# Kernel tuning notes

Measured on AMD Instinct MI355X. Metric: run time of the kernel, lower is better.

The kernel has to match this reference:

```python
import jax, jax.numpy as jnp
import numpy as np

N = 100_000   # num nodes
E = 1_600_000 # num edges
C = 128       # in_channels == hidden_channels
L = 3         # n_layers
EPS = 1e-5    # BatchNorm eps (torch default)


def bn(h, g, b, m, v):
    # BatchNorm1d in eval mode: running stats
    return (h - m) * jax.lax.rsqrt(v + EPS) * g + b


def sage_layer(h, src, dst, Wl_i, bl_i, Wr_i):
    # mean aggregation of incoming neighbor messages (PyG SAGEConv default)
    msg = h[src]                                                   # [E, C] gather
    agg = jax.ops.segment_sum(msg, dst, num_segments=N)            # [N, C]
    cnt = jax.ops.segment_sum(jnp.ones((src.shape[0],), h.dtype), dst, num_segments=N)
    agg = agg / jnp.maximum(cnt, 1.0)[:, None]
    return agg @ Wl_i + bl_i + h @ Wr_i                            # lin_l(agg) + lin_r(x)


def setup_inputs() -> dict:
    key = jax.random.key(0)
    ks = jax.random.split(key, 32)
    s = 0.05
    d = {}
    d["x"] = jax.random.normal(ks[0], (N, C), jnp.float32)
    d["edge_index"] = jax.random.randint(ks[1], (2, E), 0, N, dtype=jnp.int32)
    d["batch_size"] = 50_000
    d["Wl"] = jax.random.normal(ks[2], (L, C, C), jnp.float32) * s
    d["bl"] = jax.random.normal(ks[3], (L, C), jnp.float32) * s
    d["Wr"] = jax.random.normal(ks[4], (L, C, C), jnp.float32) * s
    d["bn_g"] = jax.random.uniform(ks[5], (L, C), jnp.float32, 0.5, 1.5)
    d["bn_b"] = jax.random.normal(ks[6], (L, C), jnp.float32) * s
    d["bn_m"] = jax.random.normal(ks[7], (L, C), jnp.float32) * s
    d["bn_v"] = jax.random.uniform(ks[8], (L, C), jnp.float32, 0.5, 1.5)
    d["cW1"] = jax.random.normal(ks[9], (C, C), jnp.float32) * s
    d["cb1"] = jax.random.normal(ks[10], (C,), jnp.float32) * s
    d["cg1"] = jax.random.uniform(ks[11], (C,), jnp.float32, 0.5, 1.5)
    d["cbe1"] = jax.random.normal(ks[12], (C,), jnp.float32) * s
    d["cm1"] = jax.random.normal(ks[13], (C,), jnp.float32) * s
    d["cv1"] = jax.random.uniform(ks[14], (C,), jnp.float32, 0.5, 1.5)
    d["cW2"] = jax.random.normal(ks[15], (C, C // 2), jnp.float32) * s
    d["cb2"] = jax.random.normal(ks[16], (C // 2,), jnp.float32) * s
    d["cg2"] = jax.random.uniform(ks[17], (C // 2,), jnp.float32, 0.5, 1.5)
    d["cbe2"] = jax.random.normal(ks[18], (C // 2,), jnp.float32) * s
    d["cm2"] = jax.random.normal(ks[19], (C // 2,), jnp.float32) * s
    d["cv2"] = jax.random.uniform(ks[20], (C // 2,), jnp.float32, 0.5, 1.5)
    d["cW3"] = jax.random.normal(ks[21], (C // 2, 1), jnp.float32) * s
    d["cb3"] = jax.random.normal(ks[22], (1,), jnp.float32) * s
    return d


def reference(x, edge_index, batch_size, Wl, bl, Wr, bn_g, bn_b, bn_m, bn_v,
              cW1, cb1, cg1, cbe1, cm1, cv1,
              cW2, cb2, cg2, cbe2, cm2, cv2, cW3, cb3):
    src, dst = edge_index[0], edge_index[1]
    h = x
    for l in range(L):  # small fixed layer count
        h = bn(jax.nn.relu(sage_layer(h, src, dst, Wl[l], bl[l], Wr[l])),
               bn_g[l], bn_b[l], bn_m[l], bn_v[l])
        # dropout is identity in eval mode
    h = h[:batch_size]                                             # [B, C] seed nodes
    h = jax.nn.relu(bn(h @ cW1 + cb1, cg1, cbe1, cm1, cv1))
    h = jax.nn.relu(bn(h @ cW2 + cb2, cg2, cbe2, cm2, cv2))
    return (h @ cW3 + cb3)[:, 0]                                   # [B]
```

## Files before the change

### kernel.cpp

```cpp
#include <hip/hip_runtime.h>

#define N_NODES 100000
#define N_EDGES 1600000
#define CDIM    128
#define BATCH   50000
#define NLAYERS 3
#define EPS_BN  1e-5f
#define LPAD    136

#define NBUCK   512
#define BW      196
#define EPB     4096
#define NEB     ((N_EDGES + EPB - 1) / EPB)
#define EBCAP   3584

#define ECAP    704

#define BBLK3   ((BATCH + 31) / 32)

typedef __attribute__((ext_vector_type(8))) short short8;
typedef __attribute__((ext_vector_type(4))) float floatx4;
typedef __attribute__((ext_vector_type(2))) float floatx2;

__device__ __forceinline__ unsigned short f2bf(float f) {
    unsigned int u = __float_as_uint(f);
    u = u + 0x7FFFu + ((u >> 16) & 1u);
    return (unsigned short)(u >> 16);
}
__device__ __forceinline__ unsigned int pk2(float lo, float hi) {
    return (unsigned int)f2bf(lo) | ((unsigned int)f2bf(hi) << 16);
}

__device__ __forceinline__ floatx2 fp8x2_lo(unsigned int u) {
    return __builtin_amdgcn_cvt_pk_f32_fp8((int)u, false);
}
__device__ __forceinline__ floatx2 fp8x2_hi(unsigned int u) {
    return __builtin_amdgcn_cvt_pk_f32_fp8((int)u, true);
}
__device__ __forceinline__ unsigned int f32x4_to_fp8(float f0, float f1, float f2, float f3) {
    int w = __builtin_amdgcn_cvt_pk_fp8_f32(f0, f1, 0, false);
    w = __builtin_amdgcn_cvt_pk_fp8_f32(f2, f3, w, true);
    return (unsigned int)w;
}

__device__ __forceinline__ void acc8(uint2 u, floatx2& a01, floatx2& a23,
                                     floatx2& a45, floatx2& a67) {
    a01 = a01 + fp8x2_lo(u.x);
    a23 = a23 + fp8x2_hi(u.x);
    a45 = a45 + fp8x2_lo(u.y);
    a67 = a67 + fp8x2_hi(u.y);
}
__device__ __forceinline__ void acc8w(uint2 u, float w, floatx2& a01, floatx2& a23,
                                      floatx2& a45, floatx2& a67) {
    floatx2 wv; wv.x = w; wv.y = w;
    a01 = fp8x2_lo(u.x) * wv + a01;
    a23 = fp8x2_hi(u.x) * wv + a23;
    a45 = fp8x2_lo(u.y) * wv + a45;
    a67 = fp8x2_hi(u.y) * wv + a67;
}

#define OFF_HB0   6400000
#define OFF_HB1   12800000
#define OFF_SC    19200000
#define OFF_RP    19201152
#define OFF_BCNT  19301184
#define OFF_ELIST 19302752
#define OFF_EBUF  20902752
#define OFF_WCAT  22737760
#define OFF_WH1   22786912
#define OFF_WH2   22795104
#define OFF_XQ    22800000
#define OFF_HQ0   26000000
#define OFF_HQ1   29200000

#define XBLK 12500
#define WBLK 384
#define HBLK 96
#define SETUP_BLKS (XBLK + WBLK + HBLK + 1)
__global__ __launch_bounds__(256) void setup_fill(
        const float* __restrict__ x,
        const float* __restrict__ Wl, const float* __restrict__ Wr,
        const float* __restrict__ cW1, const float* __restrict__ cW2,
        const float* __restrict__ g, const float* __restrict__ b,
        const float* __restrict__ m, const float* __restrict__ v,
        const float* __restrict__ cg1, const float* __restrict__ cbe1,
        const float* __restrict__ cm1, const float* __restrict__ cv1,
        const float* __restrict__ cg2, const float* __restrict__ cbe2,
        const float* __restrict__ cm2, const float* __restrict__ cv2,
        const int* __restrict__ ei,
        int* __restrict__ bcnt,
        unsigned int* __restrict__ ebuf,
        float* __restrict__ ws) {
    __shared__ unsigned int st[EPB];
    __shared__ unsigned short sb[EPB];
    __shared__ int lh[NBUCK];
    __shared__ int gb[NBUCK];
    __shared__ int lc[NBUCK];

    int blk = blockIdx.x;
    int tid = threadIdx.x;
    unsigned short* xb = (unsigned short*)ws;

    if (blk < XBLK) {
        int i = blk * 256 + tid;
        float4 vv = ((const float4*)x)[i];
        ushort4 o;
        o.x = f2bf(vv.x); o.y = f2bf(vv.y); o.z = f2bf(vv.z); o.w = f2bf(vv.w);
        ((ushort4*)xb)[i] = o;
        unsigned int* xq = (unsigned int*)(ws + OFF_XQ);
        xq[i] = f32x4_to_fp8(vv.x, vv.y, vv.z, vv.w);
        return;
    }
    if (blk < XBLK + WBLK) {
        unsigned short* wcat = (unsigned short*)(ws + OFF_WCAT);
        int i = (blk - XBLK) * 256 + tid;
        int l = i >> 15;
        int n = (i >> 8) & 127;
        int k = i & 255;
        float w = (k < CDIM) ? Wl[((size_t)l * CDIM + k) * CDIM + n]
                             : Wr[((size_t)l * CDIM + (k - CDIM)) * CDIM + n];
        wcat[i] = f2bf(w);
        return;
    }
    if (blk < XBLK + WBLK + HBLK) {
        unsigned short* wh1 = (unsigned short*)(ws + OFF_WH1);
        unsigned short* wh2 = (unsigned short*)(ws + OFF_WH2);
        int i = (blk - XBLK - WBLK) * 256 + tid;
        if (i < 128 * 128) {
            int n = i >> 7, k = i & 127;
            wh1[i] = f2bf(cW1[k * 128 + n]);
        } else if (i < 128 * 128 + 64 * 128) {
            int j = i - 128 * 128;
            int n = j >> 7, k = j & 127;
            wh2[j] = f2bf(cW2[k * 64 + n]);
        }
        return;
    }
    if (blk == XBLK + WBLK + HBLK) {
        float* sc = ws + OFF_SC;
        for (int i = tid; i < NLAYERS * CDIM; i += 256) {
            float s = g[i] * rsqrtf(v[i] + EPS_BN);
            sc[i] = s;
            sc[NLAYERS * CDIM + i] = b[i] - m[i] * s;
        }
        if (tid < CDIM) {
            float s = cg1[tid] * rsqrtf(cv1[tid] + EPS_BN);
            sc[768 + tid] = s;
            sc[896 + tid] = cbe1[tid] - cm1[tid] * s;
        }
        if (tid < 64) {
            float s = cg2[tid] * rsqrtf(cv2[tid] + EPS_BN);
            sc[1024 + tid] = s;
            sc[1088 + tid] = cbe2[tid] - cm2[tid] * s;
        }
        return;
    }

    int fb = blk - SETUP_BLKS;
    for (int t = tid; t < NBUCK; t += 256) { lh[t] = 0; lc[t] = 0; }
    __syncthreads();
    int base = fb * EPB;
    int cnt = min(EPB, N_EDGES - base);
    for (int k = tid; k < cnt / 4; k += 256) {
        int4 s4 = ((const int4*)(ei + base))[k];
        int4 d4 = ((const int4*)(ei + N_EDGES + base))[k];
        int i0 = k * 4;
#pragma unroll
        for (int q = 0; q < 4; ++q) {
            int s = (q == 0) ? s4.x : (q == 1) ? s4.y : (q == 2) ? s4.z : s4.w;
            int d = (q == 0) ? d4.x : (q == 1) ? d4.y : (q == 2) ? d4.z : d4.w;
            int bk = (unsigned)d / BW;
            int ld = d - bk * BW;
            st[i0 + q] = (unsigned)s | ((unsigned)ld << 17);
            sb[i0 + q] = (unsigned short)bk;
            atomicAdd(&lh[bk], 1);
        }
    }
    __syncthreads();
    for (int t = tid; t < NBUCK; t += 256) {
        int c = lh[t];
        gb[t] = c ? (t * EBCAP + atomicAdd(&bcnt[t], c)) : 0;
    }
    __syncthreads();
    for (int i = tid; i < cnt; i += 256) {
        int bk = sb[i];
        int pos = gb[bk] + atomicAdd(&lc[bk], 1);
        ebuf[pos] = st[i];
    }
}

__global__ __launch_bounds__(256) void bucket_csr(const unsigned int* __restrict__ ebuf,
                                                  const int* __restrict__ bcnt,
                                                  int* __restrict__ elist,
                                                  int* __restrict__ rowptr) {
    __shared__ int sbb[NBUCK];
    __shared__ unsigned int st[EBCAP];
    __shared__ int out[EBCAP];
    __shared__ int h[256], sscan[256], pre[256], cur[256];
    int b = blockIdx.x;
    int tid = threadIdx.x;
    int cnt = min(bcnt[b], EBCAP);

    sbb[tid] = bcnt[tid];
    sbb[tid + 256] = bcnt[tid + 256];
    h[tid] = 0; cur[tid] = 0;
    __syncthreads();
    for (int off = 1; off < NBUCK; off <<= 1) {
        int v0 = (tid >= off) ? sbb[tid - off] : 0;
        int t2 = tid + 256;
        int v1 = sbb[t2 - off];
        __syncthreads();
        sbb[tid] += v0;
        sbb[t2] += v1;
        __syncthreads();
    }
    int obase = (b == 0) ? 0 : sbb[b - 1];

    int ebase = b * EBCAP;
    for (int i = tid; i < cnt; i += 256) {
        unsigned int u = ebuf[ebase + i];
        st[i] = u;
        atomicAdd(&h[u >> 17], 1);
    }
    __syncthreads();
    sscan[tid] = h[tid];
    __syncthreads();
    for (int off = 1; off < 256; off <<= 1) {
        int v = (tid >= off) ? sscan[tid - off] : 0;
        __syncthreads();
        sscan[tid] += v;
        __syncthreads();
    }
    pre[tid] = sscan[tid] - h[tid];
    __syncthreads();
    for (int i = tid; i < cnt; i += 256) {
        unsigned int u = st[i];
        int ld = u >> 17;
        int pos = pre[ld] + atomicAdd(&cur[ld], 1);
        out[pos] = (int)(u & 0x1FFFFu);
    }
    __syncthreads();
    for (int i = tid; i < cnt; i += 256) elist[obase + i] = out[i];
    int gn = b * BW + tid;
    if (tid < BW && gn < N_NODES) rowptr[gn] = obase + pre[tid];
    if (b == 0 && tid == 0) rowptr[N_NODES] = N_EDGES;
}

__global__ __launch_bounds__(256, 6) void sage_fused(const int* __restrict__ rowptr,
                                                     const int* __restrict__ elist,
                                                     const unsigned short* __restrict__ hin,
                                                     const unsigned char* __restrict__ hinq,
                                                     unsigned short* __restrict__ hout,
                                                     unsigned char* __restrict__ houtq,
                                                     int wq,
                                                     const unsigned short* __restrict__ wcat,
                                                     const float* __restrict__ bl,
                                                     const float* __restrict__ scale,
                                                     const float* __restrict__ shift,
                                                     const unsigned short* __restrict__ wh1,
                                                     const unsigned short* __restrict__ wh2,
                                                     const float* __restrict__ cb1,
                                                     const float* __restrict__ s1,
                                                     const float* __restrict__ t1,
                                                     const float* __restrict__ cb2,
                                                     const float* __restrict__ s2,
                                                     const float* __restrict__ t2,
                                                     const float* __restrict__ W3,
                                                     const float* __restrict__ b3,
                                                     float* __restrict__ out) {
    __shared__ unsigned short sA[32][LPAD];
    __shared__ unsigned short sH[32][LPAD];
    __shared__ int selist[ECAP + 8];
    __shared__ int srp[33];
    __shared__ float sP[4][32];
    __shared__ float sw3[64];

    int row0 = blockIdx.x * 32;
    int tid = threadIdx.x;
    int lane = tid & 31;
    int grp = tid >> 5;
    int sub = lane >> 4;
    int li  = lane & 15;
    int li8 = li * 8;

    int beg0 = rowptr[row0];
    int end0 = rowptr[row0 + 32];
    int ecnt = min(end0 - beg0, ECAP);
    for (int i = tid; i < ecnt + 8; i += 256)
        selist[i] = (i < ecnt) ? elist[beg0 + i] : 0;
    if (tid < 33) srp[tid] = rowptr[row0 + tid];
    if (out && tid < 64) sw3[tid] = W3[tid];
    for (int it = 0; it < 4; ++it) {
        int idx = it * 256 + tid;
        int r = idx >> 5;
        int c4 = idx & 31;
        uint2 u = ((const uint2*)(hin + (size_t)(row0 + r) * CDIM))[c4];
        *((uint2*)&sH[r][c4 * 4]) = u;
    }
    __syncthreads();

    for (int rr = 0; rr < 4; ++rr) {
        int r = rr * 8 + grp;
        int beg = srp[r];
        int end = srp[r + 1];
        bool all_cached = (end - beg0) <= ecnt;
        floatx2 a01 = (floatx2)0.f, a23 = (floatx2)0.f,
                a45 = (floatx2)0.f, a67 = (floatx2)0.f;

        for (int j = beg + sub * 8; j < end; j += 16) {
            int lj = j - beg0;
            int s0, s1q, s2q, s3q, s4q, s5q, s6q, s7q;
            if (all_cached || (lj + 8 <= ecnt)) {
                s0  = selist[lj];     s1q = selist[lj + 1];
                s2q = selist[lj + 2]; s3q = selist[lj + 3];
                s4q = selist[lj + 4]; s5q = selist[lj + 5];
                s6q = selist[lj + 6]; s7q = selist[lj + 7];
            } else {
                s0  = elist[j];     s1q = elist[j + 1];
                s2q = elist[j + 2]; s3q = elist[j + 3];
                s4q = elist[j + 4]; s5q = elist[j + 5];
                s6q = elist[j + 6]; s7q = elist[j + 7];
            }
            bool p1 = (j + 1 < end), p2 = (j + 2 < end), p3 = (j + 3 < end),
                 p4 = (j + 4 < end), p5 = (j + 5 < end), p6 = (j + 6 < end),
                 p7 = (j + 7 < end);
            s1q = p1 ? s1q : 0; s2q = p2 ? s2q : 0; s3q = p3 ? s3q : 0;
            s4q = p4 ? s4q : 0; s5q = p5 ? s5q : 0; s6q = p6 ? s6q : 0;
            s7q = p7 ? s7q : 0;
            uint2 u0 = *((const uint2*)(hinq + (unsigned)((s0  << 7) + li8)));
            uint2 u1 = *((const uint2*)(hinq + (unsigned)((s1q << 7) + li8)));
            uint2 u2 = *((const uint2*)(hinq + (unsigned)((s2q << 7) + li8)));
            uint2 u3 = *((const uint2*)(hinq + (unsigned)((s3q << 7) + li8)));
            uint2 u4 = *((const uint2*)(hinq + (unsigned)((s4q << 7) + li8)));
            uint2 u5 = *((const uint2*)(hinq + (unsigned)((s5q << 7) + li8)));
            uint2 u6 = *((const uint2*)(hinq + (unsigned)((s6q << 7) + li8)));
            uint2 u7 = *((const uint2*)(hinq + (unsigned)((s7q << 7) + li8)));
            acc8(u0, a01, a23, a45, a67);
            acc8w(u1, p1 ? 1.f : 0.f, a01, a23, a45, a67);
            acc8w(u2, p2 ? 1.f : 0.f, a01, a23, a45, a67);
            acc8w(u3, p3 ? 1.f : 0.f, a01, a23, a45, a67);
            acc8w(u4, p4 ? 1.f : 0.f, a01, a23, a45, a67);
            acc8w(u5, p5 ? 1.f : 0.f, a01, a23, a45, a67);
            acc8w(u6, p6 ? 1.f : 0.f, a01, a23, a45, a67);
            acc8w(u7, p7 ? 1.f : 0.f, a01, a23, a45, a67);
        }

        float a0 = a01.x, a1 = a01.y, a2 = a23.x, a3 = a23.y,
              a4 = a45.x, a5 = a45.y, a6 = a67.x, a7 = a67.y;
        a0 += __shfl_xor(a0, 16); a1 += __shfl_xor(a1, 16);
        a2 += __shfl_xor(a2, 16); a3 += __shfl_xor(a3, 16);
        a4 += __shfl_xor(a4, 16); a5 += __shfl_xor(a5, 16);
        a6 += __shfl_xor(a6, 16); a7 += __shfl_xor(a7, 16);
        if (sub == 0) {
            float rin = 1.0f / fmaxf((float)(end - beg), 1.0f);
            uint4 o;
            o.x = pk2(a0 * rin, a1 * rin);
            o.y = pk2(a2 * rin, a3 * rin);
            o.z = pk2(a4 * rin, a5 * rin);
            o.w = pk2(a6 * rin, a7 * rin);
            *((uint4*)&sA[r][li8]) = o;
        }
    }
    __syncthreads();

    int wave = tid >> 6;
    int wl   = tid & 63;
    int ln16 = wl & 15;
    int quad = wl >> 4;

    floatx4 acc[2][2];
#pragma unroll
    for (int mt = 0; mt < 2; ++mt)
#pragma unroll
        for (int nt = 0; nt < 2; ++nt) acc[mt][nt] = (floatx4)0.0f;

    const unsigned short* wbase = wcat + ((size_t)(wave * 32 + ln16) * 256 + quad * 8);

#pragma unroll
    for (int kb = 0; kb < 8; ++kb) {
        int koff = (kb & 3) * 32 + quad * 8;
        const unsigned short* sbuf = (kb < 4) ? &sA[0][0] : &sH[0][0];
        short8 a0 = *((const short8*)(sbuf + (ln16)      * LPAD + koff));
        short8 a1 = *((const short8*)(sbuf + (ln16 + 16) * LPAD + koff));
        short8 b0 = *((const short8*)(wbase + kb * 32));
        short8 b1 = *((const short8*)(wbase + 16 * 256 + kb * 32));
        acc[0][0] = __builtin_amdgcn_mfma_f32_16x16x32_bf16(a0, b0, acc[0][0], 0, 0, 0);
        acc[1][0] = __builtin_amdgcn_mfma_f32_16x16x32_bf16(a1, b0, acc[1][0], 0, 0, 0);
        acc[0][1] = __builtin_amdgcn_mfma_f32_16x16x32_bf16(a0, b1, acc[0][1], 0, 0, 0);
        acc[1][1] = __builtin_amdgcn_mfma_f32_16x16x32_bf16(a1, b1, acc[1][1], 0, 0, 0);
    }

    __syncthreads();
#pragma unroll
    for (int nt = 0; nt < 2; ++nt) {
        int col = wave * 32 + nt * 16 + ln16;
        float bb = bl[col];
        float ss = scale[col];
        float tt = shift[col];
#pragma unroll
        for (int mt = 0; mt < 2; ++mt) {
#pragma unroll
            for (int r = 0; r < 4; ++r) {
                float v = fmaxf(acc[mt][nt][r] + bb, 0.0f) * ss + tt;
                sA[mt * 16 + quad * 4 + r][col] = f2bf(v);
            }
        }
    }
    __syncthreads();

    if (!out) {
#pragma unroll
        for (int it = 0; it < 2; ++it) {
            int idx = it * 256 + tid;
            int r = idx >> 4;
            int c = idx & 15;
            uint4 u = *((const uint4*)&sA[r][c * 8]);
            *((uint4*)(hout + (size_t)(row0 + r) * CDIM + c * 8)) = u;
            if (wq) {
                float f0 = __uint_as_float(u.x << 16), f1 = __uint_as_float(u.x & 0xFFFF0000u);
                float f2 = __uint_as_float(u.y << 16), f3 = __uint_as_float(u.y & 0xFFFF0000u);
                float f4 = __uint_as_float(u.z << 16), f5 = __uint_as_float(u.z & 0xFFFF0000u);
                float f6 = __uint_as_float(u.w << 16), f7 = __uint_as_float(u.w & 0xFFFF0000u);
                uint2 q;
                q.x = f32x4_to_fp8(f0, f1, f2, f3);
                q.y = f32x4_to_fp8(f4, f5, f6, f7);
                *((uint2*)(houtq + (size_t)(row0 + r) * 128 + c * 8)) = q;
            }
        }
        return;
    }

    floatx4 h1[2][2];
#pragma unroll
    for (int mt = 0; mt < 2; ++mt) { h1[mt][0] = (floatx4)0.0f; h1[mt][1] = (floatx4)0.0f; }
    const unsigned short* w1a = wh1 + (size_t)(wave * 32 + ln16) * 128 + quad * 8;
    const unsigned short* w1b = w1a + 16 * 128;
#pragma unroll
    for (int kb = 0; kb < 4; ++kb) {
        int koff = kb * 32 + quad * 8;
        short8 b0 = *((const short8*)(w1a + kb * 32));
        short8 b1 = *((const short8*)(w1b + kb * 32));
#pragma unroll
        for (int mt = 0; mt < 2; ++mt) {
            short8 af = *((const short8*)(&sA[mt * 16 + ln16][koff]));
            h1[mt][0] = __builtin_amdgcn_mfma_f32_16x16x32_bf16(af, b0, h1[mt][0], 0, 0, 0);
            h1[mt][1] = __builtin_amdgcn_mfma_f32_16x16x32_bf16(af, b1, h1[mt][1], 0, 0, 0);
        }
    }
    __syncthreads();
#pragma unroll
    for (int nt = 0; nt < 2; ++nt) {
        int col = wave * 32 + nt * 16 + ln16;
        float bb = cb1[col], ss = s1[col], tt = t1[col];
#pragma unroll
        for (int mt = 0; mt < 2; ++mt) {
#pragma unroll
            for (int r = 0; r < 4; ++r) {
                float v = fmaxf((h1[mt][nt][r] + bb) * ss + tt, 0.0f);
                sA[mt * 16 + quad * 4 + r][col] = f2bf(v);
            }
        }
    }
    __syncthreads();

    floatx4 h2[2];
    h2[0] = (floatx4)0.0f; h2[1] = (floatx4)0.0f;
    const unsigned short* w2a = wh2 + (size_t)(wave * 16 + ln16) * 128 + quad * 8;
#pragma unroll
    for (int kb = 0; kb < 4; ++kb) {
        int koff = kb * 32 + quad * 8;
        short8 b0 = *((const short8*)(w2a + kb * 32));
#pragma unroll
        for (int mt = 0; mt < 2; ++mt) {
            short8 af = *((const short8*)(&sA[mt * 16 + ln16][koff]));
            h2[mt] = __builtin_amdgcn_mfma_f32_16x16x32_bf16(af, b0, h2[mt], 0, 0, 0);
        }
    }
    {
        int col = wave * 16 + ln16;
        float bb = cb2[col], ss = s2[col], tt = t2[col];
        float w3v = sw3[col];
#pragma unroll
        for (int mt = 0; mt < 2; ++mt) {
#pragma unroll
            for (int r = 0; r < 4; ++r) {
                float v = fmaxf((h2[mt][r] + bb) * ss + tt, 0.0f) * w3v;
                v += __shfl_xor(v, 1);
                v += __shfl_xor(v, 2);
                v += __shfl_xor(v, 4);
                v += __shfl_xor(v, 8);
                if (ln16 == 0) sP[wave][mt * 16 + quad * 4 + r] = v;
            }
        }
    }
    __syncthreads();
    if (tid < 32) {
        int row = row0 + tid;
        if (row < BATCH)
            out[row] = sP[0][tid] + sP[1][tid] + sP[2][tid] + sP[3][tid] + b3[0];
    }
}

extern "C" void kernel_launch(void* const* d_in, const int* in_sizes, int n_in,
                              void* d_out, int out_size, void* d_ws, size_t ws_size,
                              hipStream_t stream) {
    const float* x    = (const float*)d_in[0];
    const int*   ei   = (const int*)d_in[1];
    const float* Wl   = (const float*)d_in[3];
    const float* bl   = (const float*)d_in[4];
    const float* Wr   = (const float*)d_in[5];
    const float* bn_g = (const float*)d_in[6];
    const float* bn_b = (const float*)d_in[7];
    const float* bn_m = (const float*)d_in[8];
    const float* bn_v = (const float*)d_in[9];
    const float* cW1  = (const float*)d_in[10];
    const float* cb1  = (const float*)d_in[11];
    const float* cg1  = (const float*)d_in[12];
    const float* cbe1 = (const float*)d_in[13];
    const float* cm1  = (const float*)d_in[14];
    const float* cv1  = (const float*)d_in[15];
    const float* cW2  = (const float*)d_in[16];
    const float* cb2  = (const float*)d_in[17];
    const float* cg2  = (const float*)d_in[18];
    const float* cbe2 = (const float*)d_in[19];
    const float* cm2  = (const float*)d_in[20];
    const float* cv2  = (const float*)d_in[21];
    const float* cW3  = (const float*)d_in[22];
    const float* cb3  = (const float*)d_in[23];

    float* ws  = (float*)d_ws;
    unsigned short* xb  = (unsigned short*)ws;
    unsigned short* hb0 = (unsigned short*)(ws + OFF_HB0);
    unsigned short* hb1 = (unsigned short*)(ws + OFF_HB1);
    float* sc    = ws + OFF_SC;
    int* rowptr  = (int*)(ws + OFF_RP);
    int* bcnt    = (int*)(ws + OFF_BCNT);
    int* elist   = (int*)(ws + OFF_ELIST);
    unsigned int* ebuf = (unsigned int*)(ws + OFF_EBUF);
    unsigned short* wcat = (unsigned short*)(ws + OFF_WCAT);
    unsigned short* wh1  = (unsigned short*)(ws + OFF_WH1);
    unsigned short* wh2  = (unsigned short*)(ws + OFF_WH2);
    unsigned char* xq  = (unsigned char*)(ws + OFF_XQ);
    unsigned char* hq0 = (unsigned char*)(ws + OFF_HQ0);
    unsigned char* hq1 = (unsigned char*)(ws + OFF_HQ1);

    hipMemsetAsync(bcnt, 0, NBUCK * sizeof(int), stream);

    setup_fill<<<SETUP_BLKS + NEB, 256, 0, stream>>>(
        x, Wl, Wr, cW1, cW2,
        bn_g, bn_b, bn_m, bn_v,
        cg1, cbe1, cm1, cv1,
        cg2, cbe2, cm2, cv2,
        ei, bcnt, ebuf, ws);

    bucket_csr<<<NBUCK, 256, 0, stream>>>(ebuf, bcnt, elist, rowptr);

    sage_fused<<<N_NODES / 32, 256, 0, stream>>>(
        rowptr, elist, xb, xq, hb0, hq0, 1,
        wcat, bl, sc, sc + 384,
        nullptr, nullptr, nullptr, nullptr, nullptr,
        nullptr, nullptr, nullptr, nullptr, nullptr, nullptr);
    sage_fused<<<N_NODES / 32, 256, 0, stream>>>(
        rowptr, elist, hb0, hq0, hb1, hq1, 1,
        wcat + (size_t)CDIM * 256, bl + CDIM, sc + CDIM, sc + 384 + CDIM,
        nullptr, nullptr, nullptr, nullptr, nullptr,
        nullptr, nullptr, nullptr, nullptr, nullptr, nullptr);
    sage_fused<<<BBLK3, 256, 0, stream>>>(
        rowptr, elist, hb1, hq1, hb0, hq0, 0,
        wcat + (size_t)2 * CDIM * 256, bl + 2 * CDIM, sc + 2 * CDIM, sc + 384 + 2 * CDIM,
        wh1, wh2,
        cb1, sc + 768, sc + 896,
        cb2, sc + 1024, sc + 1088,
        cW3, cb3, (float*)d_out);
}
```

Measured before the change: 327.7 us.

## Merge CSR bucketing into setup kernel via spin-wait and trim layer-2 bf16 stores

Folds the bucket_csr pass into the preprocessing kernel: edge-binning blocks increment a global done counter, and CSR-building blocks spin until all binning blocks finish before they build rowptr and elist. This removes one kernel launch and its boundary. Layer 2 also writes bf16 activations only for rows that layer 3 processes, which cuts write traffic. The spin-wait relies on the binning blocks being scheduled first and could deadlock if block dispatch order is not guaranteed.

```diff
diff --git a/kernel.cpp b/kernel.cpp
--- a/kernel.cpp
+++ b/kernel.cpp
@@ -17,6 +17,7 @@
 #define ECAP    704
 
 #define BBLK3   ((BATCH + 31) / 32)
+#define L3ROWS  (BBLK3 * 32)
 
 typedef __attribute__((ext_vector_type(8))) short short8;
 typedef __attribute__((ext_vector_type(4))) float floatx4;
@@ -76,8 +77,10 @@
 #define XBLK 12500
 #define WBLK 384
 #define HBLK 96
-#define SETUP_BLKS (XBLK + WBLK + HBLK + 1)
-__global__ __launch_bounds__(256) void setup_fill(
+#define CONV_BLKS (XBLK + WBLK + HBLK + 1)
+#define MEGA_BLKS (NEB + NBUCK + CONV_BLKS)
+
+__global__ __launch_bounds__(256) void mega_pre(
         const float* __restrict__ x,
         const float* __restrict__ Wl, const float* __restrict__ Wr,
         const float* __restrict__ cW1, const float* __restrict__ cW2,
@@ -90,19 +93,126 @@
         const int* __restrict__ ei,
         int* __restrict__ bcnt,
         unsigned int* __restrict__ ebuf,
+        int* __restrict__ elist,
+        int* __restrict__ rowptr,
         float* __restrict__ ws) {
-    __shared__ unsigned int st[EPB];
-    __shared__ unsigned short sb[EPB];
-    __shared__ int lh[NBUCK];
-    __shared__ int gb[NBUCK];
-    __shared__ int lc[NBUCK];
-
+    __shared__ int smem[8704];
     int blk = blockIdx.x;
     int tid = threadIdx.x;
+    int* doneCnt = bcnt + NBUCK;
+
+    if (blk < NEB) {
+        unsigned int* st = (unsigned int*)smem;
+        unsigned short* sb = (unsigned short*)(smem + 4096);
+        int* lh = smem + 4096 + 2048;
+        int* gb = lh + NBUCK;
+        int* lc = gb + NBUCK;
+        for (int t = tid; t < NBUCK; t += 256) { lh[t] = 0; lc[t] = 0; }
+        __syncthreads();
+        int base = blk * EPB;
+        int cnt = min(EPB, N_EDGES - base);
+        for (int k = tid; k < cnt / 4; k += 256) {
+            int4 s4 = ((const int4*)(ei + base))[k];
+            int4 d4 = ((const int4*)(ei + N_EDGES + base))[k];
+            int i0 = k * 4;
+#pragma unroll
+            for (int q = 0; q < 4; ++q) {
+                int s = (q == 0) ? s4.x : (q == 1) ? s4.y : (q == 2) ? s4.z : s4.w;
+                int d = (q == 0) ? d4.x : (q == 1) ? d4.y : (q == 2) ? d4.z : d4.w;
+                int bk = (unsigned)d / BW;
+                int ld = d - bk * BW;
+                st[i0 + q] = (unsigned)s | ((unsigned)ld << 17);
+                sb[i0 + q] = (unsigned short)bk;
+                atomicAdd(&lh[bk], 1);
+            }
+        }
+        __syncthreads();
+        for (int t = tid; t < NBUCK; t += 256) {
+            int c = lh[t];
+            gb[t] = c ? (t * EBCAP + atomicAdd(&bcnt[t], c)) : 0;
+        }
+        __syncthreads();
+        for (int i = tid; i < cnt; i += 256) {
+            int bk = sb[i];
+            int pos = gb[bk] + atomicAdd(&lc[bk], 1);
+            ebuf[pos] = st[i];
+        }
+        __syncthreads();
+        __threadfence();
+        if (tid == 0) atomicAdd(doneCnt, 1);
+        return;
+    }
+
+    if (blk < NEB + NBUCK) {
+        int bkt = blk - NEB;
+        if (tid == 0) {
+            while (atomicAdd(doneCnt, 0) < NEB)
+                __builtin_amdgcn_s_sleep(32);
+        }
+        __syncthreads();
+        __threadfence();
+
+        int* sbb = smem;
+        unsigned int* st = (unsigned int*)(smem + NBUCK);
+        int* out = smem + NBUCK + EBCAP;
+        int* h     = out + EBCAP;
+        int* sscan = h + 256;
+        int* pre   = sscan + 256;
+        int* cur   = pre + 256;
+
+        int cnt = min(bcnt[bkt], EBCAP);
+
+        sbb[tid] = bcnt[tid];
+        sbb[tid + 256] = bcnt[tid + 256];
+        h[tid] = 0; cur[tid] = 0;
+        __syncthreads();
+        for (int off = 1; off < NBUCK; off <<= 1) {
+            int v0 = (tid >= off) ? sbb[tid - off] : 0;
+            int t2 = tid + 256;
+            int v1 = sbb[t2 - off];
+            __syncthreads();
+            sbb[tid] += v0;
+            sbb[t2] += v1;
+            __syncthreads();
+        }
+        int obase = (bkt == 0) ? 0 : sbb[bkt - 1];
+
+        int ebase = bkt * EBCAP;
+        for (int i = tid; i < cnt; i += 256) {
+            unsigned int u = ebuf[ebase + i];
+            st[i] = u;
+            atomicAdd(&h[u >> 17], 1);
+        }
+        __syncthreads();
+        sscan[tid] = h[tid];
+        __syncthreads();
+        for (int off = 1; off < 256; off <<= 1) {
+            int v = (tid >= off) ? sscan[tid - off] : 0;
+            __syncthreads();
+            sscan[tid] += v;
+            __syncthreads();
+        }
+        pre[tid] = sscan[tid] - h[tid];
+        __syncthreads();
+        for (int i = tid; i < cnt; i += 256) {
+            unsigned int u = st[i];
+            int ld = u >> 17;
+            int pos = pre[ld] + atomicAdd(&cur[ld], 1);
+            out[pos] = (int)(u & 0x1FFFFu);
+        }
+        __syncthreads();
+        for (int i = tid; i < cnt; i += 256) elist[obase + i] = out[i];
+        int gn = bkt * BW + tid;
+        if (tid < BW && gn < N_NODES) rowptr[gn] = obase + pre[tid];
+        if (bkt == 0 && tid == 0) rowptr[N_NODES] = N_EDGES;
+        return;
+    }
+
+    int cb = blk - NEB - NBUCK;
     unsigned short* xb = (unsigned short*)ws;
 
-    if (blk < XBLK) {
-        int i = blk * 256 + tid;
+    if (cb < XBLK) {
+        int i = cb * 256 + tid;
         float4 vv = ((const float4*)x)[i];
         ushort4 o;
         o.x = f2bf(vv.x); o.y = f2bf(vv.y); o.z = f2bf(vv.z); o.w = f2bf(vv.w);
@@ -111,9 +221,9 @@
         xq[i] = f32x4_to_fp8(vv.x, vv.y, vv.z, vv.w);
         return;
     }
-    if (blk < XBLK + WBLK) {
+    if (cb < XBLK + WBLK) {
         unsigned short* wcat = (unsigned short*)(ws + OFF_WCAT);
-        int i = (blk - XBLK) * 256 + tid;
+        int i = (cb - XBLK) * 256 + tid;
         int l = i >> 15;
         int n = (i >> 8) & 127;
         int k = i & 255;
@@ -122,10 +232,10 @@
         wcat[i] = f2bf(w);
         return;
     }
-    if (blk < XBLK + WBLK + HBLK) {
+    if (cb < XBLK + WBLK + HBLK) {
         unsigned short* wh1 = (unsigned short*)(ws + OFF_WH1);
         unsigned short* wh2 = (unsigned short*)(ws + OFF_WH2);
-        int i = (blk - XBLK - WBLK) * 256 + tid;
+        int i = (cb - XBLK - WBLK) * 256 + tid;
         if (i < 128 * 128) {
             int n = i >> 7, k = i & 127;
             wh1[i] = f2bf(cW1[k * 128 + n]);
@@ -136,114 +246,22 @@
         }
         return;
     }
-    if (blk == XBLK + WBLK + HBLK) {
-        float* sc = ws + OFF_SC;
-        for (int i = tid; i < NLAYERS * CDIM; i += 256) {
-            float s = g[i] * rsqrtf(v[i] + EPS_BN);
-            sc[i] = s;
-            sc[NLAYERS * CDIM + i] = b[i] - m[i] * s;
-        }
-        if (tid < CDIM) {
-            float s = cg1[tid] * rsqrtf(cv1[tid] + EPS_BN);
-            sc[768 + tid] = s;
-            sc[896 + tid] = cbe1[tid] - cm1[tid] * s;
-        }
-        if (tid < 64) {
-            float s = cg2[tid] * rsqrtf(cv2[tid] + EPS_BN);
-            sc[1024 + tid] = s;
-            sc[1088 + tid] = cbe2[tid] - cm2[tid] * s;
-        }
-        return;
-    }
-
-    int fb = blk - SETUP_BLKS;
-    for (int t = tid; t < NBUCK; t += 256) { lh[t] = 0; lc[t] = 0; }
-    __syncthreads();
-    int base = fb * EPB;
-    int cnt = min(EPB, N_EDGES - base);
-    for (int k = tid; k < cnt / 4; k += 256) {
-        int4 s4 = ((const int4*)(ei + base))[k];
-        int4 d4 = ((const int4*)(ei + N_EDGES + base))[k];
-        int i0 = k * 4;
-#pragma unroll
-        for (int q = 0; q < 4; ++q) {
-            int s = (q == 0) ? s4.x : (q == 1) ? s4.y : (q == 2) ? s4.z : s4.w;
-            int d = (q == 0) ? d4.x : (q == 1) ? d4.y : (q == 2) ? d4.z : d4.w;
-            int bk = (unsigned)d / BW;
-            int ld = d - bk * BW;
-            st[i0 + q] = (unsigned)s | ((unsigned)ld << 17);
-            sb[i0 + q] = (unsigned short)bk;
-            atomicAdd(&lh[bk], 1);
-        }
-    }
-    __syncthreads();
-    for (int t = tid; t < NBUCK; t += 256) {
-        int c = lh[t];
-        gb[t] = c ? (t * EBCAP + atomicAdd(&bcnt[t], c)) : 0;
-    }
-    __syncthreads();
-    for (int i = tid; i < cnt; i += 256) {
-        int bk = sb[i];
-        int pos = gb[bk] + atomicAdd(&lc[bk], 1);
-        ebuf[pos] = st[i];
-    }
-}
-
-__global__ __launch_bounds__(256) void bucket_csr(const unsigned int* __restrict__ ebuf,
-                                                  const int* __restrict__ bcnt,
-                                                  int* __restrict__ elist,
-                                                  int* __restrict__ rowptr) {
-    __shared__ int sbb[NBUCK];
-    __shared__ unsigned int st[EBCAP];
-    __shared__ int out[EBCAP];
-    __shared__ int h[256], sscan[256], pre[256], cur[256];
-    int b = blockIdx.x;
-    int tid = threadIdx.x;
-    int cnt = min(bcnt[b], EBCAP);
-
-    sbb[tid] = bcnt[tid];
-    sbb[tid + 256] = bcnt[tid + 256];
-    h[tid] = 0; cur[tid] = 0;
-    __syncthreads();
-    for (int off = 1; off < NBUCK; off <<= 1) {
-        int v0 = (tid >= off) ? sbb[tid - off] : 0;
-        int t2 = tid + 256;
-        int v1 = sbb[t2 - off];
-        __syncthreads();
-        sbb[tid] += v0;
-        sbb[t2] += v1;
-        __syncthreads();
-    }
-    int obase = (b == 0) ? 0 : sbb[b - 1];
-
-    int ebase = b * EBCAP;
-    for (int i = tid; i < cnt; i += 256) {
-        unsigned int u = ebuf[ebase + i];
-        st[i] = u;
-        atomicAdd(&h[u >> 17], 1);
-    }
-    __syncthreads();
-    sscan[tid] = h[tid];
-    __syncthreads();
-    for (int off = 1; off < 256; off <<= 1) {
-        int v = (tid >= off) ? sscan[tid - off] : 0;
-        __syncthreads();
-        sscan[tid] += v;
-        __syncthreads();
-    }
-    pre[tid] = sscan[tid] - h[tid];
-    __syncthreads();
-    for (int i = tid; i < cnt; i += 256) {
-        unsigned int u = st[i];
-        int ld = u >> 17;
-        int pos = pre[ld] + atomicAdd(&cur[ld], 1);
-        out[pos] = (int)(u & 0x1FFFFu);
-    }
-    __syncthreads();
-    for (int i = tid; i < cnt; i += 256) elist[obase + i] = out[i];
-    int gn = b * BW + tid;
-    if (tid < BW && gn < N_NODES) rowptr[gn] = obase + pre[tid];
-    if (b == 0 && tid == 0) rowptr[N_NODES] = N_EDGES;
+    float* sc = ws + OFF_SC;
+    for (int i = tid; i < NLAYERS * CDIM; i += 256) {
+        float s = g[i] * rsqrtf(v[i] + EPS_BN);
+        sc[i] = s;
+        sc[NLAYERS * CDIM + i] = b[i] - m[i] * s;
+    }
+    if (tid < CDIM) {
+        float s = cg1[tid] * rsqrtf(cv1[tid] + EPS_BN);
+        sc[768 + tid] = s;
+        sc[896 + tid] = cbe1[tid] - cm1[tid] * s;
+    }
+    if (tid < 64) {
+        float s = cg2[tid] * rsqrtf(cv2[tid] + EPS_BN);
+        sc[1024 + tid] = s;
+        sc[1088 + tid] = cbe2[tid] - cm2[tid] * s;
+    }
 }
 
 __global__ __launch_bounds__(256, 6) void sage_fused(const int* __restrict__ rowptr,
@@ -253,6 +271,7 @@
                                                      unsigned short* __restrict__ hout,
                                                      unsigned char* __restrict__ houtq,
                                                      int wq,
+                                                     int bf16_limit,
                                                      const unsigned short* __restrict__ wcat,
                                                      const float* __restrict__ bl,
                                                      const float* __restrict__ scale,
@@ -415,7 +434,8 @@
             int r = idx >> 4;
             int c = idx & 15;
             uint4 u = *((const uint4*)&sA[r][c * 8]);
-            *((uint4*)(hout + (size_t)(row0 + r) * CDIM + c * 8)) = u;
+            if (row0 + r < bf16_limit)
+                *((uint4*)(hout + (size_t)(row0 + r) * CDIM + c * 8)) = u;
             if (wq) {
                 float f0 = __uint_as_float(u.x << 16), f1 = __uint_as_float(u.x & 0xFFFF0000u);
                 float f2 = __uint_as_float(u.y << 16), f3 = __uint_as_float(u.y & 0xFFFF0000u);
@@ -544,29 +564,27 @@
     unsigned char* hq0 = (unsigned char*)(ws + OFF_HQ0);
     unsigned char* hq1 = (unsigned char*)(ws + OFF_HQ1);
 
-    hipMemsetAsync(bcnt, 0, NBUCK * sizeof(int), stream);
-
-    setup_fill<<<SETUP_BLKS + NEB, 256, 0, stream>>>(
+    hipMemsetAsync(bcnt, 0, (NBUCK + 1) * sizeof(int), stream);
+
+    mega_pre<<<MEGA_BLKS, 256, 0, stream>>>(
         x, Wl, Wr, cW1, cW2,
         bn_g, bn_b, bn_m, bn_v,
         cg1, cbe1, cm1, cv1,
         cg2, cbe2, cm2, cv2,
-        ei, bcnt, ebuf, ws);
-
-    bucket_csr<<<NBUCK, 256, 0, stream>>>(ebuf, bcnt, elist, rowptr);
+        ei, bcnt, ebuf, elist, rowptr, ws);
 
     sage_fused<<<N_NODES / 32, 256, 0, stream>>>(
-        rowptr, elist, xb, xq, hb0, hq0, 1,
+        rowptr, elist, xb, xq, hb0, hq0, 1, N_NODES,
         wcat, bl, sc, sc + 384,
         nullptr, nullptr, nullptr, nullptr, nullptr,
         nullptr, nullptr, nullptr, nullptr, nullptr, nullptr);
     sage_fused<<<N_NODES / 32, 256, 0, stream>>>(
-        rowptr, elist, hb0, hq0, hb1, hq1, 1,
+        rowptr, elist, hb0, hq0, hb1, hq1, 1, L3ROWS,
         wcat + (size_t)CDIM * 256, bl + CDIM, sc + CDIM, sc + 384 + CDIM,
         nullptr, nullptr, nullptr, nullptr, nullptr,
         nullptr, nullptr, nullptr, nullptr, nullptr, nullptr);
     sage_fused<<<BBLK3, 256, 0, stream>>>(
-        rowptr, elist, hb1, hq1, hb0, hq0, 0,
+        rowptr, elist, hb1, hq1, hb0, hq0, 0, 0,
         wcat + (size_t)2 * CDIM * 256, bl + 2 * CDIM, sc + 2 * CDIM, sc + 384 + 2 * CDIM,
         wh1, wh2,
         cb1, sc + 768, sc + 896,
```

Result: slower. 459.2 us (+40.1%).

## Split setup kernel into grid-stride convert and bucket fill; skip unneeded bf16 stores

Applied to the files above, without the earlier changes.

The combined setup kernel becomes two kernels: a grid-stride conversion kernel with far fewer blocks, and a separate edge bucketing kernel. Layer 2 now writes bf16 rows only for the first L3ROWS nodes, since layer 3 reads full-precision self features only for the batch rows and uses fp8 for neighbours. This cuts redundant global writes, but the extra launch and the loss of overlap between conversion and bucketing inside one grid could cost time.

```diff
diff --git a/kernel.cpp b/kernel.cpp
--- a/kernel.cpp
+++ b/kernel.cpp
@@ -17,6 +17,7 @@
 #define ECAP    704
 
 #define BBLK3   ((BATCH + 31) / 32)
+#define L3ROWS  (BBLK3 * 32)
 
 typedef __attribute__((ext_vector_type(8))) short short8;
 typedef __attribute__((ext_vector_type(4))) float floatx4;
@@ -73,11 +74,12 @@
 #define OFF_HQ0   26000000
 #define OFF_HQ1   29200000
 
-#define XBLK 12500
+#define CVX  2048
 #define WBLK 384
 #define HBLK 96
-#define SETUP_BLKS (XBLK + WBLK + HBLK + 1)
-__global__ __launch_bounds__(256) void setup_fill(
+#define CONV_BLKS (CVX + WBLK + HBLK + 1)
+
+__global__ __launch_bounds__(256) void convert_all(
         const float* __restrict__ x,
         const float* __restrict__ Wl, const float* __restrict__ Wr,
         const float* __restrict__ cW1, const float* __restrict__ cW2,
@@ -87,33 +89,26 @@
         const float* __restrict__ cm1, const float* __restrict__ cv1,
         const float* __restrict__ cg2, const float* __restrict__ cbe2,
         const float* __restrict__ cm2, const float* __restrict__ cv2,
-        const int* __restrict__ ei,
-        int* __restrict__ bcnt,
-        unsigned int* __restrict__ ebuf,
         float* __restrict__ ws) {
-    __shared__ unsigned int st[EPB];
-    __shared__ unsigned short sb[EPB];
-    __shared__ int lh[NBUCK];
-    __shared__ int gb[NBUCK];
-    __shared__ int lc[NBUCK];
-
     int blk = blockIdx.x;
     int tid = threadIdx.x;
     unsigned short* xb = (unsigned short*)ws;
 
-    if (blk < XBLK) {
-        int i = blk * 256 + tid;
-        float4 vv = ((const float4*)x)[i];
-        ushort4 o;
-        o.x = f2bf(vv.x); o.y = f2bf(vv.y); o.z = f2bf(vv.z); o.w = f2bf(vv.w);
-        ((ushort4*)xb)[i] = o;
+    if (blk < CVX) {
+        const int total = N_NODES * CDIM / 4;
         unsigned int* xq = (unsigned int*)(ws + OFF_XQ);
-        xq[i] = f32x4_to_fp8(vv.x, vv.y, vv.z, vv.w);
+        for (int i = blk * 256 + tid; i < total; i += CVX * 256) {
+            float4 vv = ((const float4*)x)[i];
+            ushort4 o;
+            o.x = f2bf(vv.x); o.y = f2bf(vv.y); o.z = f2bf(vv.z); o.w = f2bf(vv.w);
+            ((ushort4*)xb)[i] = o;
+            xq[i] = f32x4_to_fp8(vv.x, vv.y, vv.z, vv.w);
+        }
         return;
     }
-    if (blk < XBLK + WBLK) {
+    if (blk < CVX + WBLK) {
         unsigned short* wcat = (unsigned short*)(ws + OFF_WCAT);
-        int i = (blk - XBLK) * 256 + tid;
+        int i = (blk - CVX) * 256 + tid;
         int l = i >> 15;
         int n = (i >> 8) & 127;
         int k = i & 255;
@@ -122,10 +117,10 @@
         wcat[i] = f2bf(w);
         return;
     }
-    if (blk < XBLK + WBLK + HBLK) {
+    if (blk < CVX + WBLK + HBLK) {
         unsigned short* wh1 = (unsigned short*)(ws + OFF_WH1);
         unsigned short* wh2 = (unsigned short*)(ws + OFF_WH2);
-        int i = (blk - XBLK - WBLK) * 256 + tid;
+        int i = (blk - CVX - WBLK) * 256 + tid;
         if (i < 128 * 128) {
             int n = i >> 7, k = i & 127;
             wh1[i] = f2bf(cW1[k * 128 + n]);
@@ -136,30 +131,36 @@
         }
         return;
     }
-    if (blk == XBLK + WBLK + HBLK) {
-        float* sc = ws + OFF_SC;
-        for (int i = tid; i < NLAYERS * CDIM; i += 256) {
-            float s = g[i] * rsqrtf(v[i] + EPS_BN);
-            sc[i] = s;
-            sc[NLAYERS * CDIM + i] = b[i] - m[i] * s;
-        }
-        if (tid < CDIM) {
-            float s = cg1[tid] * rsqrtf(cv1[tid] + EPS_BN);
-            sc[768 + tid] = s;
-            sc[896 + tid] = cbe1[tid] - cm1[tid] * s;
-        }
-        if (tid < 64) {
-            float s = cg2[tid] * rsqrtf(cv2[tid] + EPS_BN);
-            sc[1024 + tid] = s;
-            sc[1088 + tid] = cbe2[tid] - cm2[tid] * s;
-        }
-        return;
-    }
-
-    int fb = blk - SETUP_BLKS;
+    float* sc = ws + OFF_SC;
+    for (int i = tid; i < NLAYERS * CDIM; i += 256) {
+        float s = g[i] * rsqrtf(v[i] + EPS_BN);
+        sc[i] = s;
+        sc[NLAYERS * CDIM + i] = b[i] - m[i] * s;
+    }
+    if (tid < CDIM) {
+        float s = cg1[tid] * rsqrtf(cv1[tid] + EPS_BN);
+        sc[768 + tid] = s;
+        sc[896 + tid] = cbe1[tid] - cm1[tid] * s;
+    }
+    if (tid < 64) {
+        float s = cg2[tid] * rsqrtf(cv2[tid] + EPS_BN);
+        sc[1024 + tid] = s;
+        sc[1088 + tid] = cbe2[tid] - cm2[tid] * s;
+    }
+}
+
+__global__ __launch_bounds__(256) void bucket_fill(const int* __restrict__ ei,
+                                                   int* __restrict__ bcnt,
+                                                   unsigned int* __restrict__ ebuf) {
+    __shared__ unsigned int st[EPB];
+    __shared__ unsigned short sb[EPB];
+    __shared__ int lh[NBUCK];
+    __shared__ int gb[NBUCK];
+    __shared__ int lc[NBUCK];
+    int tid = threadIdx.x;
     for (int t = tid; t < NBUCK; t += 256) { lh[t] = 0; lc[t] = 0; }
     __syncthreads();
-    int base = fb * EPB;
+    int base = blockIdx.x * EPB;
     int cnt = min(EPB, N_EDGES - base);
     for (int k = tid; k < cnt / 4; k += 256) {
         int4 s4 = ((const int4*)(ei + base))[k];
@@ -253,6 +254,7 @@
                                                      unsigned short* __restrict__ hout,
                                                      unsigned char* __restrict__ houtq,
                                                      int wq,
+                                                     int bf16_limit,
                                                      const unsigned short* __restrict__ wcat,
                                                      const float* __restrict__ bl,
                                                      const float* __restrict__ scale,
@@ -415,7 +417,8 @@
             int r = idx >> 4;
             int c = idx & 15;
             uint4 u = *((const uint4*)&sA[r][c * 8]);
-            *((uint4*)(hout + (size_t)(row0 + r) * CDIM + c * 8)) = u;
+            if (row0 + r < bf16_limit)
+                *((uint4*)(hout + (size_t)(row0 + r) * CDIM + c * 8)) = u;
             if (wq) {
                 float f0 = __uint_as_float(u.x << 16), f1 = __uint_as_float(u.x & 0xFFFF0000u);
                 float f2 = __uint_as_float(u.y << 16), f3 = __uint_as_float(u.y & 0xFFFF0000u);
@@ -546,27 +549,27 @@
 
     hipMemsetAsync(bcnt, 0, NBUCK * sizeof(int), stream);
 
-    setup_fill<<<SETUP_BLKS + NEB, 256, 0, stream>>>(
+    convert_all<<<CONV_BLKS, 256, 0, stream>>>(
         x, Wl, Wr, cW1, cW2,
         bn_g, bn_b, bn_m, bn_v,
         cg1, cbe1, cm1, cv1,
-        cg2, cbe2, cm2, cv2,
-        ei, bcnt, ebuf, ws);
-
+        cg2, cbe2, cm2, cv2, ws);
+
+    bucket_fill<<<NEB, 256, 0, stream>>>(ei, bcnt, ebuf);
     bucket_csr<<<NBUCK, 256, 0, stream>>>(ebuf, bcnt, elist, rowptr);
 
     sage_fused<<<N_NODES / 32, 256, 0, stream>>>(
-        rowptr, elist, xb, xq, hb0, hq0, 1,
+        rowptr, elist, xb, xq, hb0, hq0, 1, N_NODES,
         wcat, bl, sc, sc + 384,
         nullptr, nullptr, nullptr, nullptr, nullptr,
         nullptr, nullptr, nullptr, nullptr, nullptr, nullptr);
     sage_fused<<<N_NODES / 32, 256, 0, stream>>>(
-        rowptr, elist, hb0, hq0, hb1, hq1, 1,
+        rowptr, elist, hb0, hq0, hb1, hq1, 1, L3ROWS,
         wcat + (size_t)CDIM * 256, bl + CDIM, sc + CDIM, sc + 384 + CDIM,
         nullptr, nullptr, nullptr, nullptr, nullptr,
         nullptr, nullptr, nullptr, nullptr, nullptr, nullptr);
     sage_fused<<<BBLK3, 256, 0, stream>>>(
-        rowptr, elist, hb1, hq1, hb0, hq0, 0,
+        rowptr, elist, hb1, hq1, hb0, hq0, 0, 0,
         wcat + (size_t)2 * CDIM * 256, bl + 2 * CDIM, sc + 2 * CDIM, sc + 384 + 2 * CDIM,
         wh1, wh2,
         cb1, sc + 768, sc + 896,
```

Measured after the change: 331.2 us. Within noise of the previous version (+1.1%).
